# Kernel optimization log

Hardware: AMD Instinct MI355X
Metric: run time of the kernel (lower is better)

The kernel has to match this reference:

```python
import jax, jax.numpy as jnp
import numpy as np

IN_DIM = 16384
OUT_DIM = 8192
BATCH = 1024
MASK_DENSITY = 0.05


def setup_inputs() -> dict:
    key = jax.random.key(0)
    k_x, k_w, k_b, k_m = jax.random.split(key, 4)
    x = jax.random.normal(k_x, (BATCH, IN_DIM), dtype=jnp.float32)
    # kaiming_uniform(a=sqrt(5)) == uniform(-1/sqrt(in), 1/sqrt(in))
    bound = 1.0 / np.sqrt(IN_DIM)
    weights = jax.random.uniform(k_w, (OUT_DIM, IN_DIM), dtype=jnp.float32,
                                 minval=-bound, maxval=bound)
    bias = jax.random.uniform(k_b, (OUT_DIM,), dtype=jnp.float32,
                              minval=-bound, maxval=bound)
    mask = (jax.random.uniform(k_m, (OUT_DIM, IN_DIM)) < MASK_DENSITY).astype(jnp.float32)
    return {"x": x, "weights": weights, "bias": bias, "mask": mask}


def reference(x, weights, bias, mask):
    # output = x @ (weights * mask)^T + bias   (F.linear semantics)
    masked_w = weights * mask  # [out, in]
    return jnp.einsum('bi,oi->bo', x, masked_w) + bias
```

## Files before the change

kernel.cpp:

```cpp
#include <hip/hip_runtime.h>


#define IN_DIM 16384
#define OUT_DIM 8192
#define BATCH 1024

#define BM 256
#define BN 256
#define BK 64
#define KSPLIT 2
#define K_HALF (IN_DIM / KSPLIT)
#define NT_K (K_HALF / BK)
#define NT256 (OUT_DIM / BN)
#define MT256 (BATCH / BM)

typedef __attribute__((ext_vector_type(8))) short bf16x8;
typedef __attribute__((ext_vector_type(4))) float f32x4;
typedef __attribute__((ext_vector_type(8))) unsigned short u16x8;

__device__ __forceinline__ unsigned short f2bf(float f) {
  unsigned int u = __float_as_uint(f);
  return (unsigned short)((u + 0x7fffu + ((u >> 16) & 1u)) >> 16);
}

#define GL16(g, l)                                                \
  __builtin_amdgcn_global_load_lds(                               \
      (const __attribute__((address_space(1))) void*)(g),         \
      (__attribute__((address_space(3))) void*)(l), 16, 0, 0)

__global__ __launch_bounds__(256) void prep_w_kernel(
    const f32x4* __restrict__ w, const f32x4* __restrict__ m,
    u16x8* __restrict__ out, int n8) {
  int i = blockIdx.x * blockDim.x + threadIdx.x;
  int stride = gridDim.x * blockDim.x;
  for (; i < n8; i += stride) {
    f32x4 w0 = __builtin_nontemporal_load(&w[2 * i]);
    f32x4 w1 = __builtin_nontemporal_load(&w[2 * i + 1]);
    f32x4 m0 = __builtin_nontemporal_load(&m[2 * i]);
    f32x4 m1 = __builtin_nontemporal_load(&m[2 * i + 1]);
    u16x8 o;
    o[0] = f2bf(w0[0] * m0[0]);
    o[1] = f2bf(w0[1] * m0[1]);
    o[2] = f2bf(w0[2] * m0[2]);
    o[3] = f2bf(w0[3] * m0[3]);
    o[4] = f2bf(w1[0] * m1[0]);
    o[5] = f2bf(w1[1] * m1[1]);
    o[6] = f2bf(w1[2] * m1[2]);
    o[7] = f2bf(w1[3] * m1[3]);
    __builtin_nontemporal_store(o, &out[i]);
  }
}

__global__ __launch_bounds__(256) void prep_x_kernel(
    const f32x4* __restrict__ x, u16x8* __restrict__ out, int n8) {
  int i = blockIdx.x * blockDim.x + threadIdx.x;
  int stride = gridDim.x * blockDim.x;
  for (; i < n8; i += stride) {
    f32x4 v0 = __builtin_nontemporal_load(&x[2 * i]);
    f32x4 v1 = __builtin_nontemporal_load(&x[2 * i + 1]);
    u16x8 o;
    o[0] = f2bf(v0[0]);
    o[1] = f2bf(v0[1]);
    o[2] = f2bf(v0[2]);
    o[3] = f2bf(v0[3]);
    o[4] = f2bf(v1[0]);
    o[5] = f2bf(v1[1]);
    o[6] = f2bf(v1[2]);
    o[7] = f2bf(v1[3]);
    __builtin_nontemporal_store(o, &out[i]);
  }
}

__global__ __launch_bounds__(256) void reduce_kernel(
    const f32x4* __restrict__ p0, const f32x4* __restrict__ p1,
    const f32x4* __restrict__ bias4, f32x4* __restrict__ out, int n4) {
  int i = blockIdx.x * blockDim.x + threadIdx.x;
  int stride = gridDim.x * blockDim.x;
  for (; i < n4; i += stride) {
    f32x4 a = p0[i];
    f32x4 b = p1[i];
    f32x4 c = bias4[i & (OUT_DIM / 4 - 1)];
    out[i] = a + b + c;
  }
}

__global__ __launch_bounds__(1024, 4) void gemm256(
    const short* __restrict__ Ab, const short* __restrict__ Bb,
    float* __restrict__ out0, float* __restrict__ out1) {
  __shared__ short As[2][256 * 64];
  __shared__ short Bs[2][256 * 64];

  const int tid = threadIdx.x;
  const int lane = tid & 63;
  const int wv = tid >> 6;
  const int wr = wv >> 2;
  const int wc = wv & 3;
  const int fr = lane & 15;
  const int fq = lane >> 4;

  const int bid = blockIdx.x;
  const int nt = bid & (NT256 - 1);
  const int rest = bid >> 5;
  const int mt = rest >> 1;
  const int kh = rest & 1;
  const int row0 = mt * BM;
  const int col0 = nt * BN;
  const int kbase = kh * K_HALF;
  float* __restrict__ dst = kh ? out1 : out0;

  const int swz8 = ((tid & 7) ^ ((tid >> 3) & 7)) * 8;
  const short* srcA = Ab + (size_t)(row0 + (tid >> 3)) * IN_DIM + kbase + swz8;
  const short* srcB = Bb + (size_t)(col0 + (tid >> 3)) * IN_DIM + kbase + swz8;
  char* ldsA = (char*)As;
  char* ldsB = (char*)Bs;
  const int stg = wv * 1024;

#define STAGE_A(KT, SL)                                                    \
  do {                                                                     \
    GL16(srcA + (size_t)(KT)*64, ldsA + (SL)*32768 + stg);                 \
    GL16(srcA + (size_t)128 * IN_DIM + (size_t)(KT)*64,                    \
         ldsA + (SL)*32768 + 16384 + stg);                                 \
  } while (0)
#define STAGE_B(KT, SL)                                                    \
  do {                                                                     \
    GL16(srcB + (size_t)(KT)*64, ldsB + (SL)*32768 + stg);                 \
    GL16(srcB + (size_t)128 * IN_DIM + (size_t)(KT)*64,                    \
         ldsB + (SL)*32768 + 16384 + stg);                                 \
  } while (0)

  const int swzslot = (fq ^ (fr & 7)) * 16;
  const int Abase = (wr * 64 + fr) * 128 + swzslot;
  const int Bbase = (wc * 64 + fr) * 128 + swzslot;

  f32x4 acc[4][4];
#pragma unroll
  for (int i = 0; i < 4; ++i)
#pragma unroll
    for (int j = 0; j < 4; ++j) acc[i][j] = (f32x4)0.f;

  STAGE_A(0, 0);
  STAGE_B(0, 0);

#pragma unroll 1
  for (int t = 0; t < NT_K; ++t) {
    const int cur = t & 1;
    if (t + 1 < NT_K) {
      STAGE_A(t + 1, cur ^ 1);
      STAGE_B(t + 1, cur ^ 1);
      asm volatile("s_waitcnt vmcnt(4)" ::: "memory");
    } else {
      asm volatile("s_waitcnt vmcnt(0)" ::: "memory");
    }
    __builtin_amdgcn_s_barrier();

    const char* tA = (const char*)As + cur * 32768;
    const char* tB = (const char*)Bs + cur * 32768;
#pragma unroll
    for (int ks = 0; ks < 2; ++ks) {
      const int off = ks << 6;
      bf16x8 bF[4];
#pragma unroll
      for (int n = 0; n < 4; ++n)
        bF[n] = *(const bf16x8*)(tB + ((Bbase + n * 2048) ^ off));
#pragma unroll
      for (int m = 0; m < 4; ++m) {
        bf16x8 aF = *(const bf16x8*)(tA + ((Abase + m * 2048) ^ off));
#pragma unroll
        for (int n = 0; n < 4; ++n)
          acc[m][n] = __builtin_amdgcn_mfma_f32_16x16x32_bf16(aF, bF[n],
                                                              acc[m][n], 0, 0,
                                                              0);
      }
    }
    __builtin_amdgcn_s_barrier();
  }

#pragma unroll
  for (int m = 0; m < 4; ++m) {
#pragma unroll
    for (int n = 0; n < 4; ++n) {
      const int c = col0 + wc * 64 + n * 16 + fr;
      const int rb = row0 + wr * 64 + m * 16 + fq * 4;
#pragma unroll
      for (int tt = 0; tt < 4; ++tt)
        dst[(size_t)(rb + tt) * OUT_DIM + c] = acc[m][n][tt];
    }
  }
#undef STAGE_A
#undef STAGE_B
}

__global__ __launch_bounds__(256) void gemm128_fused(
    const float* __restrict__ X, const float* __restrict__ W,
    const float* __restrict__ Msk, const float* __restrict__ bias,
    float* __restrict__ out) {
  __shared__ short As[128 * 64];
  __shared__ short Bs[128 * 64];
  const int tid = threadIdx.x;
  const int lane = tid & 63;
  const int wv4 = tid >> 6;
  const int wm = wv4 >> 1;
  const int wn = wv4 & 1;
  const int fr = lane & 15;
  const int fq = lane >> 4;
  const int bid = blockIdx.x;
  const int nt = bid & 63;
  const int mt = bid >> 6;
  const int row0 = mt * 128;
  const int col0 = nt * 128;
  f32x4 acc[4][4];
#pragma unroll
  for (int i = 0; i < 4; ++i)
#pragma unroll
    for (int j = 0; j < 4; ++j) acc[i][j] = (f32x4)0.f;
  for (int kt = 0; kt < IN_DIM / 64; ++kt) {
    const int k0 = kt * 64;
    __syncthreads();
#pragma unroll
    for (int is = 0; is < 4; ++is) {
      const int e = (is * 256 + tid) * 8;
      const int r = e >> 6;
      const int kk = e & 63;
      {
        const float* src = X + (size_t)(row0 + r) * IN_DIM + k0 + kk;
        f32x4 a0 = *(const f32x4*)src;
        f32x4 a1 = *(const f32x4*)(src + 4);
        bf16x8 v;
        v[0] = (short)f2bf(a0[0]); v[1] = (short)f2bf(a0[1]);
        v[2] = (short)f2bf(a0[2]); v[3] = (short)f2bf(a0[3]);
        v[4] = (short)f2bf(a1[0]); v[5] = (short)f2bf(a1[1]);
        v[6] = (short)f2bf(a1[2]); v[7] = (short)f2bf(a1[3]);
        *(bf16x8*)&As[r * 64 + kk] = v;
      }
      {
        const float* sw = W + (size_t)(col0 + r) * IN_DIM + k0 + kk;
        const float* sm = Msk + (size_t)(col0 + r) * IN_DIM + k0 + kk;
        f32x4 w0 = *(const f32x4*)sw;
        f32x4 w1 = *(const f32x4*)(sw + 4);
        f32x4 m0 = *(const f32x4*)sm;
        f32x4 m1 = *(const f32x4*)(sm + 4);
        bf16x8 v;
        v[0] = (short)f2bf(w0[0] * m0[0]); v[1] = (short)f2bf(w0[1] * m0[1]);
        v[2] = (short)f2bf(w0[2] * m0[2]); v[3] = (short)f2bf(w0[3] * m0[3]);
        v[4] = (short)f2bf(w1[0] * m1[0]); v[5] = (short)f2bf(w1[1] * m1[1]);
        v[6] = (short)f2bf(w1[2] * m1[2]); v[7] = (short)f2bf(w1[3] * m1[3]);
        *(bf16x8*)&Bs[r * 64 + kk] = v;
      }
    }
    __syncthreads();
#pragma unroll
    for (int ks = 0; ks < 2; ++ks) {
      bf16x8 af[4], bf[4];
#pragma unroll
      for (int i = 0; i < 4; ++i)
        af[i] = *(const bf16x8*)&As[(wm * 64 + i * 16 + fr) * 64 + ks * 32 + fq * 8];
#pragma unroll
      for (int j = 0; j < 4; ++j)
        bf[j] = *(const bf16x8*)&Bs[(wn * 64 + j * 16 + fr) * 64 + ks * 32 + fq * 8];
#pragma unroll
      for (int i = 0; i < 4; ++i)
#pragma unroll
        for (int j = 0; j < 4; ++j)
          acc[i][j] = __builtin_amdgcn_mfma_f32_16x16x32_bf16(af[i], bf[j],
                                                              acc[i][j], 0, 0, 0);
    }
  }
#pragma unroll
  for (int j = 0; j < 4; ++j) {
    const int c = col0 + wn * 64 + j * 16 + fr;
    const float bv = bias[c];
#pragma unroll
    for (int i = 0; i < 4; ++i) {
      const int rb = row0 + wm * 64 + i * 16 + fq * 4;
#pragma unroll
      for (int tt = 0; tt < 4; ++tt)
        out[(size_t)(rb + tt) * OUT_DIM + c] = acc[i][j][tt] + bv;
    }
  }
}

extern "C" void kernel_launch(void* const* d_in, const int* in_sizes, int n_in,
                              void* d_out, int out_size, void* d_ws, size_t ws_size,
                              hipStream_t stream) {
  const float* x = (const float*)d_in[0];
  const float* w = (const float*)d_in[1];
  const float* bias = (const float*)d_in[2];
  const float* mask = (const float*)d_in[3];
  float* out = (float*)d_out;

  const size_t wm_elems = (size_t)OUT_DIM * IN_DIM;
  const size_t xb_elems = (size_t)BATCH * IN_DIM;
  const size_t out_elems = (size_t)BATCH * OUT_DIM;
  const size_t need_bf16 = (wm_elems + xb_elems) * sizeof(short);
  const size_t need_split = need_bf16 + out_elems * sizeof(float);

  if (ws_size >= need_split) {
    short* wmb = (short*)d_ws;
    short* xbb = wmb + wm_elems;
    float* p1 = (float*)((char*)d_ws + need_bf16);
    hipLaunchKernelGGL(prep_w_kernel, dim3(4096), dim3(256), 0, stream,
                       (const f32x4*)w, (const f32x4*)mask, (u16x8*)wmb,
                       (int)(wm_elems / 8));
    hipLaunchKernelGGL(prep_x_kernel, dim3(512), dim3(256), 0, stream,
                       (const f32x4*)x, (u16x8*)xbb, (int)(xb_elems / 8));
    hipLaunchKernelGGL(gemm256, dim3(KSPLIT * MT256 * NT256), dim3(1024), 0,
                       stream, xbb, wmb, out, p1);
    hipLaunchKernelGGL(reduce_kernel, dim3(2048), dim3(256), 0, stream,
                       (const f32x4*)out, (const f32x4*)p1,
                       (const f32x4*)bias, (f32x4*)out, (int)(out_elems / 4));
  } else {
    hipLaunchKernelGGL(gemm128_fused, dim3(512), dim3(256), 0, stream, x, w,
                       mask, bias, out);
  }
}
```

Baseline: 551.6 us.

## Replace split-K 256x256 GEMM with 128x256 tiles and fused bias epilogue

Drops the two-way K split and its separate reduction kernel. The GEMM now uses 128x256 output tiles over the full K range, which keeps the block count at 256, and adds the bias in the epilogue. This removes writing and re-reading a full fp32 partial output and one kernel launch. In exchange each block runs twice as many K iterations with fewer MFMAs per LDS load, lowering arithmetic intensity per tile and adding more A/B global traffic per output.

```diff
diff --git a/kernel.cpp b/kernel.cpp
--- a/kernel.cpp
+++ b/kernel.cpp
@@ -5,14 +5,12 @@
 #define OUT_DIM 8192
 #define BATCH 1024
 
-#define BM 256
+#define BM 128
 #define BN 256
 #define BK 64
-#define KSPLIT 2
-#define K_HALF (IN_DIM / KSPLIT)
-#define NT_K (K_HALF / BK)
-#define NT256 (OUT_DIM / BN)
-#define MT256 (BATCH / BM)
+#define NT_K (IN_DIM / BK)
+#define NTT (OUT_DIM / BN)
+#define MTT (BATCH / BM)
 
 typedef __attribute__((ext_vector_type(8))) short bf16x8;
 typedef __attribute__((ext_vector_type(4))) float f32x4;
@@ -71,23 +69,10 @@
   }
 }
 
-__global__ __launch_bounds__(256) void reduce_kernel(
-    const f32x4* __restrict__ p0, const f32x4* __restrict__ p1,
-    const f32x4* __restrict__ bias4, f32x4* __restrict__ out, int n4) {
-  int i = blockIdx.x * blockDim.x + threadIdx.x;
-  int stride = gridDim.x * blockDim.x;
-  for (; i < n4; i += stride) {
-    f32x4 a = p0[i];
-    f32x4 b = p1[i];
-    f32x4 c = bias4[i & (OUT_DIM / 4 - 1)];
-    out[i] = a + b + c;
-  }
-}
-
-__global__ __launch_bounds__(1024, 4) void gemm256(
+__global__ __launch_bounds__(1024, 4) void gemm(
     const short* __restrict__ Ab, const short* __restrict__ Bb,
-    float* __restrict__ out0, float* __restrict__ out1) {
-  __shared__ short As[2][256 * 64];
+    const float* __restrict__ bias, float* __restrict__ out) {
+  __shared__ short As[2][128 * 64];
   __shared__ short Bs[2][256 * 64];
 
   const int tid = threadIdx.x;
@@ -99,61 +84,50 @@
   const int fq = lane >> 4;
 
   const int bid = blockIdx.x;
-  const int nt = bid & (NT256 - 1);
-  const int rest = bid >> 5;
-  const int mt = rest >> 1;
-  const int kh = rest & 1;
+  const int nt = bid & (NTT - 1);
+  const int mt = bid >> 5;
   const int row0 = mt * BM;
   const int col0 = nt * BN;
-  const int kbase = kh * K_HALF;
-  float* __restrict__ dst = kh ? out1 : out0;
 
   const int swz8 = ((tid & 7) ^ ((tid >> 3) & 7)) * 8;
-  const short* srcA = Ab + (size_t)(row0 + (tid >> 3)) * IN_DIM + kbase + swz8;
-  const short* srcB = Bb + (size_t)(col0 + (tid >> 3)) * IN_DIM + kbase + swz8;
+  const short* srcA = Ab + (size_t)(row0 + (tid >> 3)) * IN_DIM + swz8;
+  const short* srcB = Bb + (size_t)(col0 + (tid >> 3)) * IN_DIM + swz8;
   char* ldsA = (char*)As;
   char* ldsB = (char*)Bs;
   const int stg = wv * 1024;
 
-#define STAGE_A(KT, SL)                                                    \
+#define STAGE(KT, SL)                                                      \
   do {                                                                     \
-    GL16(srcA + (size_t)(KT)*64, ldsA + (SL)*32768 + stg);                 \
-    GL16(srcA + (size_t)128 * IN_DIM + (size_t)(KT)*64,                    \
-         ldsA + (SL)*32768 + 16384 + stg);                                 \
-  } while (0)
-#define STAGE_B(KT, SL)                                                    \
-  do {                                                                     \
+    GL16(srcA + (size_t)(KT)*64, ldsA + (SL)*16384 + stg);                 \
     GL16(srcB + (size_t)(KT)*64, ldsB + (SL)*32768 + stg);                 \
     GL16(srcB + (size_t)128 * IN_DIM + (size_t)(KT)*64,                    \
          ldsB + (SL)*32768 + 16384 + stg);                                 \
   } while (0)
 
   const int swzslot = (fq ^ (fr & 7)) * 16;
-  const int Abase = (wr * 64 + fr) * 128 + swzslot;
+  const int Abase = (wr * 32 + fr) * 128 + swzslot;
   const int Bbase = (wc * 64 + fr) * 128 + swzslot;
 
-  f32x4 acc[4][4];
-#pragma unroll
-  for (int i = 0; i < 4; ++i)
+  f32x4 acc[2][4];
+#pragma unroll
+  for (int i = 0; i < 2; ++i)
 #pragma unroll
     for (int j = 0; j < 4; ++j) acc[i][j] = (f32x4)0.f;
 
-  STAGE_A(0, 0);
-  STAGE_B(0, 0);
+  STAGE(0, 0);
 
 #pragma unroll 1
   for (int t = 0; t < NT_K; ++t) {
     const int cur = t & 1;
     if (t + 1 < NT_K) {
-      STAGE_A(t + 1, cur ^ 1);
-      STAGE_B(t + 1, cur ^ 1);
-      asm volatile("s_waitcnt vmcnt(4)" ::: "memory");
+      STAGE(t + 1, cur ^ 1);
+      asm volatile("s_waitcnt vmcnt(3)" ::: "memory");
     } else {
       asm volatile("s_waitcnt vmcnt(0)" ::: "memory");
     }
     __builtin_amdgcn_s_barrier();
 
-    const char* tA = (const char*)As + cur * 32768;
+    const char* tA = (const char*)As + cur * 16384;
     const char* tB = (const char*)Bs + cur * 32768;
 #pragma unroll
     for (int ks = 0; ks < 2; ++ks) {
@@ -163,7 +137,7 @@
       for (int n = 0; n < 4; ++n)
         bF[n] = *(const bf16x8*)(tB + ((Bbase + n * 2048) ^ off));
 #pragma unroll
-      for (int m = 0; m < 4; ++m) {
+      for (int m = 0; m < 2; ++m) {
         bf16x8 aF = *(const bf16x8*)(tA + ((Abase + m * 2048) ^ off));
 #pragma unroll
         for (int n = 0; n < 4; ++n)
@@ -176,18 +150,18 @@
   }
 
 #pragma unroll
-  for (int m = 0; m < 4; ++m) {
+  for (int m = 0; m < 2; ++m) {
 #pragma unroll
     for (int n = 0; n < 4; ++n) {
       const int c = col0 + wc * 64 + n * 16 + fr;
-      const int rb = row0 + wr * 64 + m * 16 + fq * 4;
+      const float bv = bias[c];
+      const int rb = row0 + wr * 32 + m * 16 + fq * 4;
 #pragma unroll
       for (int tt = 0; tt < 4; ++tt)
-        dst[(size_t)(rb + tt) * OUT_DIM + c] = acc[m][n][tt];
-    }
-  }
-#undef STAGE_A
-#undef STAGE_B
+        out[(size_t)(rb + tt) * OUT_DIM + c] = acc[m][n][tt] + bv;
+    }
+  }
+#undef STAGE
 }
 
 __global__ __launch_bounds__(256) void gemm128_fused(
@@ -290,24 +264,18 @@
 
   const size_t wm_elems = (size_t)OUT_DIM * IN_DIM;
   const size_t xb_elems = (size_t)BATCH * IN_DIM;
-  const size_t out_elems = (size_t)BATCH * OUT_DIM;
   const size_t need_bf16 = (wm_elems + xb_elems) * sizeof(short);
-  const size_t need_split = need_bf16 + out_elems * sizeof(float);
-
-  if (ws_size >= need_split) {
+
+  if (ws_size >= need_bf16) {
     short* wmb = (short*)d_ws;
     short* xbb = wmb + wm_elems;
-    float* p1 = (float*)((char*)d_ws + need_bf16);
     hipLaunchKernelGGL(prep_w_kernel, dim3(4096), dim3(256), 0, stream,
                        (const f32x4*)w, (const f32x4*)mask, (u16x8*)wmb,
                        (int)(wm_elems / 8));
     hipLaunchKernelGGL(prep_x_kernel, dim3(512), dim3(256), 0, stream,
                        (const f32x4*)x, (u16x8*)xbb, (int)(xb_elems / 8));
-    hipLaunchKernelGGL(gemm256, dim3(KSPLIT * MT256 * NT256), dim3(1024), 0,
-                       stream, xbb, wmb, out, p1);
-    hipLaunchKernelGGL(reduce_kernel, dim3(2048), dim3(256), 0, stream,
-                       (const f32x4*)out, (const f32x4*)p1,
-                       (const f32x4*)bias, (f32x4*)out, (int)(out_elems / 4));
+    hipLaunchKernelGGL(gemm, dim3(MTT * NTT), dim3(1024), 0, stream, xbb, wmb,
+                       bias, out);
   } else {
     hipLaunchKernelGGL(gemm128_fused, dim3(512), dim3(256), 0, stream, x, w,
                        mask, bias, out);
```

After: 654.5 us. 1.19x slower.
